# Kernel tuning notes

Measured on AMD Instinct MI355X. Metric: run time of the kernel, lower is better.

## Reference

```python
import jax, jax.numpy as jnp
import numpy as np

N = 80000
E = 1280000
EPS = 1e-5

def _lrelu(x):
    return jax.nn.leaky_relu(x, 0.01)

def _bn(h):
    # training-mode BatchNorm1d with batch size 1: stats over the node dim; affine is identity at init
    return (h - h.mean(0)) / jnp.sqrt(h.var(0) + EPS)

def _ln(h, g, b):
    m = h.mean(-1, keepdims=True)
    v = h.var(-1, keepdims=True)
    return (h - m) / jnp.sqrt(v + EPS) * g + b

def _gcn(h, w, b, src, dst, n):
    # PyG GCNConv: add self loops, symmetric deg^-1/2 normalization, aggregate at target
    hw = h @ w.T
    loop = jnp.arange(n, dtype=src.dtype)
    s = jnp.concatenate([src, loop])
    d = jnp.concatenate([dst, loop])
    deg = jax.ops.segment_sum(jnp.ones(d.shape, hw.dtype), d, num_segments=n)
    dinv = jnp.where(deg > 0, 1.0 / jnp.sqrt(deg), 0.0)
    msg = hw[s] * (dinv[s] * dinv[d])[:, None]  # [E+N, C]
    return jax.ops.segment_sum(msg, d, num_segments=n) + b

def _tnet(x, c1w, c1b, c2w, c2b, c3w, c3b, f1w, f1b, f2w, f2b, f3w, f3b):
    h = jax.nn.relu(x @ c1w.T + c1b)          # [N,64]  (source skips bn1)
    h = jax.nn.relu(_bn(h @ c2w.T + c2b))     # [N,128]
    h = jax.nn.relu(_bn(h @ c3w.T + c3b))     # [N,1024]
    g = h.max(0)                              # global max pool -> [1024]
    g = jax.nn.relu(g @ f1w.T + f1b)
    g = jax.nn.relu(g @ f2w.T + f2b)
    iden = jnp.array([1.0, 0.0, 0.0, 0.0, 1.0, 0.0, 0.0, 0.0, 1.0], x.dtype)
    g = g @ f3w.T + f3b + iden
    return g.reshape(3, 3)

def _forward(edge_index, x, tnet_c1_w, tnet_c1_b, tnet_c2_w, tnet_c2_b, tnet_c3_w, tnet_c3_b, tnet_fc1_w, tnet_fc1_b, tnet_fc2_w, tnet_fc2_b, tnet_fc3_w, tnet_fc3_b, conv1_w, conv1_b, g1_li_w, g1_li_b, g1_gcn_w, g1_gcn_b, g1_ln_g, g1_ln_b, conv2_w, conv2_b, g2_li_w, g2_li_b, g2_gcn_w, g2_gcn_b, g2_ln_g, g2_ln_b, conv3_w, conv3_b, out_w, out_b):
    src, dst = edge_index[0], edge_index[1]
    n = x.shape[0]
    T = _tnet(x, tnet_c1_w, tnet_c1_b, tnet_c2_w, tnet_c2_b, tnet_c3_w, tnet_c3_b, tnet_fc1_w, tnet_fc1_b, tnet_fc2_w, tnet_fc2_b, tnet_fc3_w, tnet_fc3_b)
    h0 = x @ T                                  # [N,3] spatial transform
    xg = _lrelu(h0 @ conv1_w.T + conv1_b)       # [N,64] (conv1d k=1 == per-node linear)
    # Gcn_Attention 1
    nf = _lrelu(xg @ g1_li_w.T + g1_li_b)
    nf2 = _lrelu(_gcn(nf, g1_gcn_w, g1_gcn_b, src, dst, n))
    h = _ln(jnp.concatenate([nf, nf2], 1), g1_ln_g, g1_ln_b)   # [N,128]
    h = _lrelu(h @ conv2_w.T + conv2_b)
    # Gcn_Attention 2
    nf = _lrelu(h @ g2_li_w.T + g2_li_b)
    nf2 = _lrelu(_gcn(nf, g2_gcn_w, g2_gcn_b, src, dst, n))
    h = _ln(jnp.concatenate([nf, nf2], 1), g2_ln_g, g2_ln_b)   # [N,256]
    h = jnp.concatenate([h, xg], 1)                            # [N,320]
    h = _lrelu(h @ conv3_w.T + conv3_b)                        # [N,256]
    pooled = h.mean(0)                                         # global mean pool (single graph)
    feat = jnp.concatenate([jnp.broadcast_to(pooled, (n, pooled.shape[0])), xg], 1)  # [N,320]
    return feat @ out_w.T + out_b                              # [N,4]

def setup_inputs():
    ki = iter(jax.random.split(jax.random.key(0), 32))
    def W(shape):
        return jax.random.normal(next(ki), shape, jnp.float32) * (1.0 / float(np.sqrt(shape[-1])))
    z = lambda n: jnp.zeros((n,), jnp.float32)
    o = lambda n: jnp.ones((n,), jnp.float32)
    inp = {}
    inp['x'] = jax.random.normal(next(ki), (N, 3), jnp.float32)
    inp['edge_index'] = jax.random.randint(next(ki), (2, E), 0, N, dtype=jnp.int32)
    inp['tnet_c1_w'] = W((64, 3)); inp['tnet_c1_b'] = z(64)
    inp['tnet_c2_w'] = W((128, 64)); inp['tnet_c2_b'] = z(128)
    inp['tnet_c3_w'] = W((1024, 128)); inp['tnet_c3_b'] = z(1024)
    inp['tnet_fc1_w'] = W((512, 1024)); inp['tnet_fc1_b'] = z(512)
    inp['tnet_fc2_w'] = W((256, 512)); inp['tnet_fc2_b'] = z(256)
    inp['tnet_fc3_w'] = W((9, 256)); inp['tnet_fc3_b'] = z(9)
    inp['conv1_w'] = W((64, 3)); inp['conv1_b'] = z(64)
    inp['g1_li_w'] = W((64, 64)); inp['g1_li_b'] = z(64)
    inp['g1_gcn_w'] = W((64, 64)); inp['g1_gcn_b'] = z(64)
    inp['g1_ln_g'] = o(128); inp['g1_ln_b'] = z(128)
    inp['conv2_w'] = W((128, 128)); inp['conv2_b'] = z(128)
    inp['g2_li_w'] = W((128, 128)); inp['g2_li_b'] = z(128)
    inp['g2_gcn_w'] = W((128, 128)); inp['g2_gcn_b'] = z(128)
    inp['g2_ln_g'] = o(256); inp['g2_ln_b'] = z(256)
    inp['conv3_w'] = W((256, 320)); inp['conv3_b'] = z(256)
    inp['out_w'] = W((4, 320)); inp['out_b'] = z(4)
    return inp

def reference(x, edge_index, tnet_c1_w, tnet_c1_b, tnet_c2_w, tnet_c2_b, tnet_c3_w, tnet_c3_b, tnet_fc1_w, tnet_fc1_b, tnet_fc2_w, tnet_fc2_b, tnet_fc3_w, tnet_fc3_b, conv1_w, conv1_b, g1_li_w, g1_li_b, g1_gcn_w, g1_gcn_b, g1_ln_g, g1_ln_b, conv2_w, conv2_b, g2_li_w, g2_li_b, g2_gcn_w, g2_gcn_b, g2_ln_g, g2_ln_b, conv3_w, conv3_b, out_w, out_b):
    return _forward(edge_index, x, tnet_c1_w, tnet_c1_b, tnet_c2_w, tnet_c2_b, tnet_c3_w, tnet_c3_b, tnet_fc1_w, tnet_fc1_b, tnet_fc2_w, tnet_fc2_b, tnet_fc3_w, tnet_fc3_b, conv1_w, conv1_b, g1_li_w, g1_li_b, g1_gcn_w, g1_gcn_b, g1_ln_g, g1_ln_b, conv2_w, conv2_b, g2_li_w, g2_li_b, g2_gcn_w, g2_gcn_b, g2_ln_g, g2_ln_b, conv3_w, conv3_b, out_w, out_b)
```

## Files before the change

### kernel.cpp

```cpp
#include <hip/hip_runtime.h>
#include <cstddef>

#define EPSV 1e-5f

typedef __attribute__((ext_vector_type(8))) short frag8;
typedef __attribute__((ext_vector_type(4))) float f32x4;

__device__ __forceinline__ float lrelu01(float v) { return v > 0.f ? v : 0.01f * v; }
__device__ __forceinline__ void atomAddF(float* p, float v) { unsafeAtomicAdd(p, v); }
__device__ __forceinline__ unsigned fkey(float f) {
    unsigned u = __float_as_uint(f);
    return (u & 0x80000000u) ? ~u : (u | 0x80000000u);
}
__device__ __forceinline__ unsigned short f2b(float f) {
    unsigned u = __float_as_uint(f);
    unsigned r = u + 0x7fffu + ((u >> 16) & 1u);
    return (unsigned short)(r >> 16);
}
__device__ __forceinline__ float b2f(unsigned short h) {
    return __uint_as_float(((unsigned)h) << 16);
}
__device__ __forceinline__ float blo(unsigned u) { return __uint_as_float(u << 16); }
__device__ __forceinline__ float bhi(unsigned u) { return __uint_as_float(u & 0xffff0000u); }

static inline unsigned cdivu(unsigned a, unsigned b) { return (a + b - 1) / b; }

__device__ __forceinline__ void gbar(unsigned* cnt, unsigned target) {
    __syncthreads();
    if (threadIdx.x == 0) {
        __threadfence();
        atomicAdd(cnt, 1u);
        while (atomicAdd(cnt, 0u) < target) { }
        __threadfence();
    }
    __syncthreads();
}


__device__ void degrank_body(int bid, const int* __restrict__ dst, int* __restrict__ deg,
                             int* __restrict__ rank, int E) {
    int e = bid * 256 + threadIdx.x;
    if (e < E) rank[e] = atomicAdd(&deg[dst[e]], 1);
}

__device__ void scan_local_body(int bid, const int* __restrict__ deg, int* __restrict__ startv,
                                int* __restrict__ bsum, float* __restrict__ dinv, int n) {
    __shared__ int t0[256];
    int tid = threadIdx.x;
    int i = bid * 256 + tid;
    int v = (i < n) ? deg[i] : 0;
    if (i < n) dinv[i] = rsqrtf((float)(v + 1));
    t0[tid] = v;
    __syncthreads();
    for (int o = 1; o < 256; o <<= 1) {
        int add = (tid >= o) ? t0[tid - o] : 0;
        __syncthreads();
        t0[tid] += add;
        __syncthreads();
    }
    if (i < n) startv[i] = t0[tid] - v;
    if (tid == 255) bsum[bid] = t0[255];
}

__device__ void scan_bsum_body(int* __restrict__ bsum, int nb) {
    __shared__ int t0[512];
    __shared__ int t1[512];
    int tid = threadIdx.x;
    int v0 = (tid < nb) ? bsum[tid] : 0;
    int v1 = (tid + 256 < nb) ? bsum[tid + 256] : 0;
    t0[tid] = v0; t0[tid + 256] = v1;
    __syncthreads();
    int* a = t0; int* b = t1;
    for (int o = 1; o < 512; o <<= 1) {
        b[tid]       = a[tid]       + ((tid >= o)       ? a[tid - o]       : 0);
        b[tid + 256] = a[tid + 256] + ((tid + 256 >= o) ? a[tid + 256 - o] : 0);
        __syncthreads();
        int* t = a; a = b; b = t;
    }
    if (tid < nb) bsum[tid] = a[tid] - v0;
    if (tid + 256 < nb) bsum[tid + 256] = a[tid + 256] - v1;
}

__device__ void fill_body(int bid, const int* __restrict__ src, const int* __restrict__ dst,
                          const int* __restrict__ rank, const int* __restrict__ startv,
                          const int* __restrict__ bsum, int* __restrict__ csr, int E) {
    int e = bid * 256 + threadIdx.x;
    if (e < E) {
        int d = dst[e];
        csr[startv[d] + bsum[d >> 8] + rank[e]] = src[e];
    }
}


__device__ void wconv_body(int bid, const float* __restrict__ s0, const float* __restrict__ s1,
                           const float* __restrict__ s2, const float* __restrict__ s3,
                           const float* __restrict__ s4, const float* __restrict__ s5,
                           const float* __restrict__ s6, const float* __restrict__ s7,
                           unsigned short* __restrict__ dst) {
    int t = bid * 256 + threadIdx.x;
    if (t >= 278528) return;
    const float* srcs[8] = {s0, s1, s2, s3, s4, s5, s6, s7};
    const int off[9] = {0, 8192, 139264, 143360, 147456, 163840, 180224, 196608, 278528};
    int seg = 0;
    while (t >= off[seg + 1]) ++seg;
    unsigned short v = f2b(srcs[seg][t - off[seg]]);
    if (seg == 1) {
        int li = t - 8192;
        int rch = li >> 7, k = li & 127;
        int cb = rch >> 7, r = rch & 127;
        int flat = ((r >> 4) * 4 + (k >> 5)) * 64 + ((k >> 3) & 3) * 16 + (r & 15);
        dst[8192 + cb * 16384 + flat * 8 + (k & 7)] = v;
    } else {
        dst[t] = v;
    }
}

__device__ void h1_body(int bid, const float* __restrict__ x, const float* __restrict__ w,
                        const float* __restrict__ b, unsigned short* __restrict__ h1, int n) {
    int node = bid * 256 + threadIdx.x;
    if (node >= n) return;
    float x0 = x[node * 3], x1 = x[node * 3 + 1], x2 = x[node * 3 + 2];
    unsigned short* o = h1 + (size_t)node * 64;
#pragma unroll
    for (int cp = 0; cp < 8; ++cp) {
        unsigned short tmp[8];
#pragma unroll
        for (int t = 0; t < 8; ++t) {
            int c = cp * 8 + t;
            float v = x0 * w[c * 3] + x1 * w[c * 3 + 1] + x2 * w[c * 3 + 2] + b[c];
            tmp[t] = f2b(fmaxf(v, 0.f));
        }
        *(float4*)(o + cp * 8) = *(float4*)tmp;
    }
}

__device__ void prebn_body(int bid, const float* __restrict__ z, const float* __restrict__ sum2,
                           const float* __restrict__ ss2, unsigned short* __restrict__ a3f,
                           int n16, float invn) {
    int t = bid * 256 + threadIdx.x;
    if (t >= n16) return;
    int row = t >> 4, cp = t & 15;
    int c = cp * 8;
    const float* src = z + (size_t)row * 128 + c;
    float4 v0 = *(const float4*)src;
    float4 v1 = *(const float4*)(src + 4);
    float vv[8] = {v0.x, v0.y, v0.z, v0.w, v1.x, v1.y, v1.z, v1.w};
    unsigned short o[8];
#pragma unroll
    for (int i = 0; i < 8; ++i) {
        float m = sum2[c + i] * invn;
        float var = ss2[c + i] * invn - m * m;
        o[i] = f2b(fmaxf((vv[i] - m) * rsqrtf(var + EPSV), 0.f));
    }
    int tile = row >> 7, r = row & 127;
    int flat = ((r >> 4) * 4 + (cp >> 2)) * 64 + (cp & 3) * 16 + (r & 15);
    *(float4*)(a3f + (size_t)tile * 16384 + flat * 8) = *(float4*)o;
}

enum { MF_BIAS = 1, MF_LRELU = 2, MF_DINV = 4, MF_STOREF = 8, MF_STOREB = 16,
       MF_STATS = 32, MF_COLSUM = 64 };

template <int BN, int MODE>
__device__ void mgemm_body(int bx, int by,
                           const unsigned short* __restrict__ A, int lda, int K,
                           const unsigned short* __restrict__ W,
                           const float* __restrict__ bias,
                           float* __restrict__ OutF, unsigned short* __restrict__ OutB, int ldo,
                           const float* __restrict__ dinv,
                           float* __restrict__ sum_o, float* __restrict__ ss_o,
                           unsigned* __restrict__ maxk_o) {
    constexpr int BM = 128;
    constexpr int LDT = 40;
    __shared__ unsigned short As[BM * LDT];
    __shared__ unsigned short Ws[BN * LDT];
    __shared__ float redS[2 * 128];
    __shared__ unsigned redM[128];

    const int tid = threadIdx.x;
    const int wid = tid >> 6, lane = tid & 63;
    const int quad = lane >> 4, lrow = lane & 15;
    const int bn0 = bx * BM;
    const int bc0 = by * BN;

    constexpr int NI = (BN == 128) ? 4 : 2;
    constexpr int NJ = 4;
    const int wm = (BN == 128) ? (wid & 1) * 64 : wid * 32;
    const int wn = (BN == 128) ? (wid >> 1) * 64 : 0;

    if (MODE & (MF_STATS | MF_COLSUM)) {
        for (int c = tid; c < BN; c += 256) {
            redS[c] = 0.f; redS[128 + c] = 0.f; redM[c] = 0u;
        }
    }

    f32x4 acc[NI][NJ] = {};

    for (int k0 = 0; k0 < K; k0 += 32) {
#pragma unroll
        for (int h = 0; h < 2; ++h) {
            int ch = tid + h * 256;
            int row = ch >> 2, cp = ch & 3;
            const unsigned short* src = A + (size_t)(bn0 + row) * lda + k0 + cp * 8;
            *(float4*)&As[row * LDT + cp * 8] = *(const float4*)src;
        }
#pragma unroll
        for (int h = 0; h < BN / 64; ++h) {
            int ch = tid + h * 256;
            int row = ch >> 2, cp = ch & 3;
            const unsigned short* src = W + (size_t)(bc0 + row) * K + k0 + cp * 8;
            *(float4*)&Ws[row * LDT + cp * 8] = *(const float4*)src;
        }
        __syncthreads();
        frag8 af[NI], bf[NJ];
#pragma unroll
        for (int i = 0; i < NI; ++i)
            af[i] = *(const frag8*)&As[(wm + i * 16 + lrow) * LDT + quad * 8];
#pragma unroll
        for (int j = 0; j < NJ; ++j)
            bf[j] = *(const frag8*)&Ws[(wn + j * 16 + lrow) * LDT + quad * 8];
#pragma unroll
        for (int i = 0; i < NI; ++i)
#pragma unroll
            for (int j = 0; j < NJ; ++j)
                acc[i][j] = __builtin_amdgcn_mfma_f32_16x16x32_bf16(af[i], bf[j], acc[i][j], 0, 0, 0);
        __syncthreads();
    }

#pragma unroll
    for (int j = 0; j < NJ; ++j) {
        const int col = bc0 + wn + j * 16 + lrow;
        float bv = (MODE & MF_BIAS) ? bias[col] : 0.f;
        float s = 0.f, q = 0.f, m = -3.4e38f;
#pragma unroll
        for (int i = 0; i < NI; ++i) {
            const int rowb = bn0 + wm + i * 16 + quad * 4;
#pragma unroll
            for (int r = 0; r < 4; ++r) {
                float t = acc[i][j][r] + bv;
                if (MODE & MF_LRELU) t = lrelu01(t);
                if (MODE & MF_DINV) t *= dinv[rowb + r];
                if (MODE & MF_STOREF) OutF[(size_t)(rowb + r) * ldo + col] = t;
                if (MODE & MF_STOREB) OutB[(size_t)(rowb + r) * ldo + col] = f2b(t);
                s += t; q += t * t; m = fmaxf(m, t);
            }
        }
        if (MODE & (MF_STATS | MF_COLSUM)) {
            s += __shfl_xor(s, 16); s += __shfl_xor(s, 32);
            if (MODE & MF_STATS) {
                q += __shfl_xor(q, 16); q += __shfl_xor(q, 32);
                m = fmaxf(m, __shfl_xor(m, 16)); m = fmaxf(m, __shfl_xor(m, 32));
            }
            if (quad == 0) {
                int lc = wn + j * 16 + lrow;
                atomicAdd(&redS[lc], s);
                if (MODE & MF_STATS) {
                    atomicAdd(&redS[128 + lc], q);
                    atomicMax(&redM[lc], fkey(m));
                }
            }
        }
    }
    if (MODE & (MF_STATS | MF_COLSUM)) {
        __syncthreads();
        for (int c = tid; c < BN; c += 256) {
            atomAddF(&sum_o[bc0 + c], redS[c]);
            if (MODE & MF_STATS) {
                atomAddF(&ss_o[bc0 + c], redS[128 + c]);
                atomicMax(&maxk_o[bc0 + c], redM[c]);
            }
        }
    }
}

template <int BN, int MODE, int SWAP>
__launch_bounds__(256)
__global__ void k_mgemm(const unsigned short* __restrict__ A, int lda, int K,
                        const unsigned short* __restrict__ W,
                        const float* __restrict__ bias,
                        float* __restrict__ OutF, unsigned short* __restrict__ OutB, int ldo,
                        const float* __restrict__ dinv,
                        float* __restrict__ sum_o, float* __restrict__ ss_o,
                        unsigned* __restrict__ maxk_o) {
    int bx = SWAP ? blockIdx.y : blockIdx.x;
    int by = SWAP ? blockIdx.x : blockIdx.y;
    mgemm_body<BN, MODE>(bx, by, A, lda, K, W, bias, OutF, OutB, ldo, dinv, sum_o, ss_o, maxk_o);
}

__device__ void z3_body(int bid,
                        const unsigned short* __restrict__ AF,
                        const unsigned short* __restrict__ WF,
                        const float* __restrict__ bias,
                        float* __restrict__ sum_o, float* __restrict__ ss_o,
                        unsigned* __restrict__ maxk_o, int ntiles) {
    const int tid = threadIdx.x;
    const int wid = tid >> 6, lane = tid & 63;
    const int quad = lane >> 4, lrow = lane & 15;

    int w = (bid & 7) * ntiles + (bid >> 3);
    const int tile = w >> 3;
    const int cb = w & 7;
    const unsigned short* At = AF + (size_t)tile * 16384;
    const unsigned short* Wt = WF + (size_t)cb * 16384;

    const int ar = (wid & 1) * 4;
    const int wc = (wid >> 1) * 4;
    f32x4 acc[4][4] = {};
#pragma unroll
    for (int kc = 0; kc < 4; ++kc) {
        frag8 af[4], bf[4];
#pragma unroll
        for (int i = 0; i < 4; ++i)
            af[i] = *(const frag8*)&At[(((ar + i) * 4 + kc) * 64 + lane) * 8];
#pragma unroll
        for (int j = 0; j < 4; ++j)
            bf[j] = *(const frag8*)&Wt[(((wc + j) * 4 + kc) * 64 + lane) * 8];
#pragma unroll
        for (int i = 0; i < 4; ++i)
#pragma unroll
            for (int j = 0; j < 4; ++j)
                acc[i][j] = __builtin_amdgcn_mfma_f32_16x16x32_bf16(af[i], bf[j], acc[i][j], 0, 0, 0);
    }

#pragma unroll
    for (int j = 0; j < 4; ++j) {
        int c = cb * 128 + (wc + j) * 16 + lrow;
        float bv = bias[c];
        float s = 0.f, q = 0.f, m = -3.4e38f;
#pragma unroll
        for (int i = 0; i < 4; ++i)
#pragma unroll
            for (int r = 0; r < 4; ++r) {
                float t = acc[i][j][r] + bv;
                s += t; q += t * t; m = fmaxf(m, t);
            }
        s += __shfl_xor(s, 16); s += __shfl_xor(s, 32);
        q += __shfl_xor(q, 16); q += __shfl_xor(q, 32);
        m = fmaxf(m, __shfl_xor(m, 16)); m = fmaxf(m, __shfl_xor(m, 32));
        if (quad == 0) {
            atomAddF(&sum_o[c], s);
            atomAddF(&ss_o[c], q);
            atomicMax(&maxk_o[c], fkey(m));
        }
    }
}


__launch_bounds__(256)
__global__ void FK1(const int* __restrict__ dst, int* __restrict__ deg, int* __restrict__ rank,
                    int E, int EB,
                    const float* s0, const float* s1, const float* s2, const float* s3,
                    const float* s4, const float* s5, const float* s6, const float* s7,
                    unsigned short* __restrict__ WB, int WCB,
                    const float* __restrict__ x, const float* __restrict__ c1w,
                    const float* __restrict__ c1b, unsigned short* __restrict__ B1, int n) {
    int b = blockIdx.x;
    if (b < EB) { degrank_body(b, dst, deg, rank, E); return; }
    b -= EB;
    if (b < WCB) { wconv_body(b, s0, s1, s2, s3, s4, s5, s6, s7, WB); return; }
    b -= WCB;
    h1_body(b, x, c1w, c1b, B1, n);
}

__launch_bounds__(256)
__global__ void FK2(const unsigned short* __restrict__ A, int lda, int K,
                    const unsigned short* __restrict__ W, const float* __restrict__ bias,
                    float* __restrict__ OutF, int ldo,
                    float* __restrict__ sum_o, float* __restrict__ ss_o,
                    unsigned* __restrict__ maxk_o, int GXz,
                    const int* __restrict__ deg, int* __restrict__ startv,
                    int* __restrict__ bsum, float* __restrict__ dinvv, int n) {
    if ((int)blockIdx.x < GXz)
        mgemm_body<128, (MF_BIAS | MF_STOREF | MF_STATS)>(
            blockIdx.x, 0, A, lda, K, W, bias, OutF, nullptr, ldo, nullptr, sum_o, ss_o, maxk_o);
    else
        scan_local_body(blockIdx.x - GXz, deg, startv, bsum, dinvv, n);
}

__launch_bounds__(256)
__global__ void FK3(const float* __restrict__ z, const float* __restrict__ sum2,
                    const float* __restrict__ ss2, unsigned short* __restrict__ a3f,
                    int n16, float invn, int PB, int* __restrict__ bsum, int nb) {
    if ((int)blockIdx.x < PB) prebn_body(blockIdx.x, z, sum2, ss2, a3f, n16, invn);
    else scan_bsum_body(bsum, nb);
}

__launch_bounds__(256)
__global__ void FK4(const unsigned short* __restrict__ AF, const unsigned short* __restrict__ WF,
                    const float* __restrict__ bias,
                    float* __restrict__ sum_o, float* __restrict__ ss_o,
                    unsigned* __restrict__ maxk_o, int NZ, int ntiles,
                    const int* __restrict__ src, const int* __restrict__ dst,
                    const int* __restrict__ rank, const int* __restrict__ startv,
                    const int* __restrict__ bsum, int* __restrict__ csr, int E) {
    int b = blockIdx.x;
    bool dofill = (b >= NZ);
    int idx = dofill ? (b - NZ) : b;
    if (dofill) fill_body(idx, src, dst, rank, startv, bsum, csr, E);
    else        z3_body(idx, AF, WF, bias, sum_o, ss_o, maxk_o, ntiles);
}

__launch_bounds__(256)
__global__ void k_tnet(const float* __restrict__ sum3, const float* __restrict__ ss3,
                       const unsigned* __restrict__ maxk,
                       const float* __restrict__ f1w, const float* __restrict__ f1b,
                       const float* __restrict__ f2w, const float* __restrict__ f2bias,
                       const float* __restrict__ f3w, const float* __restrict__ f3b,
                       float* __restrict__ a1, float* __restrict__ a2,
                       float* __restrict__ T9,
                       unsigned* __restrict__ cnt1, unsigned* __restrict__ cnt2, float invn) {
    __shared__ float g[1024];
    __shared__ float a1s[512];
    int tid = threadIdx.x;
    int bid = blockIdx.x;
    for (int c = tid; c < 1024; c += 256) {
        float m = sum3[c] * invn;
        float var = ss3[c] * invn - m * m;
        unsigned k = maxk[c];
        unsigned u = (k & 0x80000000u) ? (k & 0x7FFFFFFFu) : ~k;
        g[c] = fmaxf((__uint_as_float(u) - m) * rsqrtf(var + EPSV), 0.f);
    }
    __syncthreads();
    {
        int row = bid * 16 + (tid >> 4);
        int part = tid & 15;
        const float* w = f1w + (size_t)row * 1024 + part * 64;
        const float* gg = g + part * 64;
        float s = 0.f;
#pragma unroll 4
        for (int k = 0; k < 64; k += 4) {
            float4 wv = *(const float4*)(w + k);
            s = fmaf(wv.x, gg[k], s);
            s = fmaf(wv.y, gg[k + 1], s);
            s = fmaf(wv.z, gg[k + 2], s);
            s = fmaf(wv.w, gg[k + 3], s);
        }
        s += __shfl_xor(s, 1); s += __shfl_xor(s, 2);
        s += __shfl_xor(s, 4); s += __shfl_xor(s, 8);
        if (part == 0) a1[row] = fmaxf(s + f1b[row], 0.f);
    }
    gbar(cnt1, 32);
    a1s[tid] = a1[tid];
    a1s[tid + 256] = a1[tid + 256];
    __syncthreads();
    {
        int row = bid * 8 + (tid >> 5);
        int part = tid & 31;
        const float* w = f2w + (size_t)row * 512 + part * 16;
        const float* aa = a1s + part * 16;
        float s = 0.f;
#pragma unroll
        for (int k = 0; k < 16; k += 4) {
            float4 wv = *(const float4*)(w + k);
            s = fmaf(wv.x, aa[k], s);
            s = fmaf(wv.y, aa[k + 1], s);
            s = fmaf(wv.z, aa[k + 2], s);
            s = fmaf(wv.w, aa[k + 3], s);
        }
        s += __shfl_xor(s, 1); s += __shfl_xor(s, 2); s += __shfl_xor(s, 4);
        s += __shfl_xor(s, 8); s += __shfl_xor(s, 16);
        if (part == 0) a2[row] = fmaxf(s + f2bias[row], 0.f);
    }
    gbar(cnt2, 32);
    if (bid == 0 && tid < 144) {
        int r = tid >> 4, kk = (tid & 15) * 16;
        const float* wr = f3w + r * 256 + kk;
        float s = 0.f;
#pragma unroll
        for (int k = 0; k < 16; ++k) s = fmaf(wr[k], a2[kk + k], s);
        s += __shfl_xor(s, 1); s += __shfl_xor(s, 2);
        s += __shfl_xor(s, 4); s += __shfl_xor(s, 8);
        if ((tid & 15) == 0) {
            s += f3b[r];
            if (r == 0 || r == 4 || r == 8) s += 1.f;
            T9[r] = s;
        }
    }
}

template <int CH>
__launch_bounds__(256)
__global__ void k_gln(const int* __restrict__ startv, const int* __restrict__ bsum,
                      const int* __restrict__ degv,
                      const int* __restrict__ csr, const unsigned short* __restrict__ q,
                      const unsigned short* __restrict__ nf, const float* __restrict__ dinv,
                      const float* __restrict__ gcn_b, const float* __restrict__ lng,
                      const float* __restrict__ lnb, unsigned short* __restrict__ outp,
                      int ldo, int n, int nd) {
    constexpr int GRP = (CH == 64) ? 8 : 4;
    constexpr int PL  = 64 / GRP;
    constexpr int TT  = 16 / GRP;
    constexpr int CPL = CH / PL;
    const int wv = threadIdx.x >> 6, lane = threadIdx.x & 63;
    const int g = lane / PL, p = lane & (PL - 1);
    int node = blockIdx.x * 4 + wv;
    if (node >= n) return;

    const unsigned short* qp = q + (size_t)p * CPL;

    float acc[CPL];
    {
        uint4 v = *(const uint4*)(qp + (size_t)node * CH);
        unsigned sv[4] = {v.x, v.y, v.z, v.w};
        if (g == 0) {
#pragma unroll
            for (int d = 0; d < 4; ++d) { acc[2 * d] = blo(sv[d]); acc[2 * d + 1] = bhi(sv[d]); }
        } else {
#pragma unroll
            for (int k = 0; k < CPL; ++k) acc[k] = 0.f;
        }
    }

    int s0 = startv[node] + bsum[node >> 8], cnt = degv[node];
    const int* cs = csr + s0;
    int sidx[TT];
#pragma unroll
    for (int t = 0; t < TT; ++t) { int j = t * GRP + g; sidx[t] = (j < cnt) ? cs[j] : nd; }
    for (int j0 = 0; j0 < cnt; j0 += 16) {
        uint4 buf[TT];
#pragma unroll
        for (int t = 0; t < TT; ++t)
            buf[t] = *(const uint4*)(qp + (size_t)(unsigned)sidx[t] * CH);
#pragma unroll
        for (int t = 0; t < TT; ++t) {
            int j = j0 + 16 + t * GRP + g;
            sidx[t] = (j < cnt) ? cs[j] : nd;
        }
#pragma unroll
        for (int t = 0; t < TT; ++t) {
            unsigned bw[4] = {buf[t].x, buf[t].y, buf[t].z, buf[t].w};
#pragma unroll
            for (int d = 0; d < 4; ++d) {
                acc[2 * d] += blo(bw[d]);
                acc[2 * d + 1] += bhi(bw[d]);
            }
        }
    }

#pragma unroll
    for (int k = 0; k < CPL; ++k) {
#pragma unroll
        for (int off = PL; off < 64; off <<= 1) acc[k] += __shfl_xor(acc[k], off);
    }

    float di = dinv[node];
    float nv[CPL], bv[CPL];
    {
        uint4 v = *(const uint4*)(nf + (size_t)node * CH + p * CPL);
        unsigned sv[4] = {v.x, v.y, v.z, v.w};
#pragma unroll
        for (int d = 0; d < 4; ++d) { nv[2 * d] = blo(sv[d]); nv[2 * d + 1] = bhi(sv[d]); }
    }
    const float* gb = gcn_b + p * CPL;
#pragma unroll
    for (int k = 0; k < CPL; ++k) bv[k] = lrelu01(di * acc[k] + gb[k]);

    float s = 0.f, ss = 0.f;
#pragma unroll
    for (int k = 0; k < CPL; ++k) { s += nv[k] + bv[k]; ss += nv[k] * nv[k] + bv[k] * bv[k]; }
#pragma unroll
    for (int off = 32; off > 0; off >>= 1) { s += __shfl_xor(s, off); ss += __shfl_xor(ss, off); }
    const float inv = 1.f / (float)(GRP * 2 * CH);
    float mu = s * inv;
    float var = ss * inv - mu * mu;
    float rsg = rsqrtf(var + EPSV);

    unsigned short* orow = outp + (size_t)node * ldo;
    if (g == 0) {
        unsigned short tmp[CPL];
        const float* lg = lng + p * CPL; const float* lb = lnb + p * CPL;
#pragma unroll
        for (int k = 0; k < CPL; ++k) tmp[k] = f2b((nv[k] - mu) * rsg * lg[k] + lb[k]);
        *(uint4*)(orow + p * CPL) = *(uint4*)tmp;
    } else if (g == 1) {
        unsigned short tmp[CPL];
        const float* lg = lng + CH + p * CPL; const float* lb = lnb + CH + p * CPL;
#pragma unroll
        for (int k = 0; k < CPL; ++k) tmp[k] = f2b((bv[k] - mu) * rsg * lg[k] + lb[k]);
        *(uint4*)(orow + CH + p * CPL) = *(uint4*)tmp;
    }
}


__launch_bounds__(256)
__global__ void k_xg2(const float* __restrict__ x, const float* __restrict__ T9,
                      const float* __restrict__ w, const float* __restrict__ b,
                      const float* __restrict__ ow,
                      unsigned short* __restrict__ xg, float* __restrict__ xdot, int n) {
    __shared__ float owS[256];
    __shared__ float T9s[9];
    int tid = threadIdx.x;
    owS[tid] = ow[(tid >> 6) * 320 + 256 + (tid & 63)];
    if (tid < 9) T9s[tid] = T9[tid];
    __syncthreads();
    int node = blockIdx.x * 256 + tid;
    if (node >= n) return;
    float x0 = x[node * 3], x1 = x[node * 3 + 1], x2 = x[node * 3 + 2];
    float h0 = x0 * T9s[0] + x1 * T9s[3] + x2 * T9s[6];
    float h1 = x0 * T9s[1] + x1 * T9s[4] + x2 * T9s[7];
    float h2 = x0 * T9s[2] + x1 * T9s[5] + x2 * T9s[8];
    unsigned short* o = xg + (size_t)node * 320;
    float d0 = 0.f, d1 = 0.f, d2 = 0.f, d3 = 0.f;
#pragma unroll
    for (int cp = 0; cp < 8; ++cp) {
        unsigned short tmp[8];
#pragma unroll
        for (int t = 0; t < 8; ++t) {
            int c = cp * 8 + t;
            float v = lrelu01(h0 * w[c * 3] + h1 * w[c * 3 + 1] + h2 * w[c * 3 + 2] + b[c]);
            tmp[t] = f2b(v);
            d0 = fmaf(v, owS[c], d0);
            d1 = fmaf(v, owS[64 + c], d1);
            d2 = fmaf(v, owS[128 + c], d2);
            d3 = fmaf(v, owS[192 + c], d3);
        }
        *(float4*)(o + cp * 8) = *(float4*)tmp;
    }
    *(float4*)(xdot + (size_t)node * 4) = make_float4(d0, d1, d2, d3);
}

template <int BN>
__launch_bounds__(256)
__global__ void k_ligc(const unsigned short* __restrict__ A, int lda, int K,
                       const unsigned short* __restrict__ Wli, const float* __restrict__ bli,
                       const unsigned short* __restrict__ Wgc, const float* __restrict__ dinv,
                       unsigned short* __restrict__ NF, int ldnf,
                       unsigned short* __restrict__ Q, int ldq) {
    constexpr int BM = 128;
    constexpr int LDT = 40;
    constexpr int LDT2 = BN + 8;
    __shared__ unsigned short SA[BM * LDT2];
    __shared__ unsigned short Ws[BN * LDT];
    __shared__ unsigned short As[BM * LDT];

    const int tid = threadIdx.x;
    const int wid = tid >> 6, lane = tid & 63;
    const int quad = lane >> 4, lrow = lane & 15;
    const int bn0 = blockIdx.x * BM;
    constexpr int NI = (BN == 128) ? 4 : 2;
    constexpr int NJ = 4;
    const int wm = (BN == 128) ? (wid & 1) * 64 : wid * 32;
    const int wn = (BN == 128) ? (wid >> 1) * 64 : 0;

    {
        f32x4 acc[NI][NJ] = {};
        for (int k0 = 0; k0 < K; k0 += 32) {
#pragma unroll
            for (int h = 0; h < 2; ++h) {
                int ch = tid + h * 256;
                int row = ch >> 2, cp = ch & 3;
                *(float4*)&As[row * LDT + cp * 8] =
                    *(const float4*)(A + (size_t)(bn0 + row) * lda + k0 + cp * 8);
            }
#pragma unroll
            for (int h = 0; h < BN / 64; ++h) {
                int ch = tid + h * 256;
                int row = ch >> 2, cp = ch & 3;
                *(float4*)&Ws[row * LDT + cp * 8] =
                    *(const float4*)(Wli + (size_t)row * K + k0 + cp * 8);
            }
            __syncthreads();
            frag8 af[NI], bf[NJ];
#pragma unroll
            for (int i = 0; i < NI; ++i)
                af[i] = *(const frag8*)&As[(wm + i * 16 + lrow) * LDT + quad * 8];
#pragma unroll
            for (int j = 0; j < NJ; ++j)
                bf[j] = *(const frag8*)&Ws[(wn + j * 16 + lrow) * LDT + quad * 8];
#pragma unroll
            for (int i = 0; i < NI; ++i)
#pragma unroll
                for (int j = 0; j < NJ; ++j)
                    acc[i][j] = __builtin_amdgcn_mfma_f32_16x16x32_bf16(af[i], bf[j], acc[i][j], 0, 0, 0);
            __syncthreads();
        }
#pragma unroll
        for (int j = 0; j < NJ; ++j) {
            const int col = wn + j * 16 + lrow;
            float bv = bli[col];
#pragma unroll
            for (int i = 0; i < NI; ++i) {
                const int rowl = wm + i * 16 + quad * 4;
#pragma unroll
                for (int r = 0; r < 4; ++r) {
                    unsigned short h = f2b(lrelu01(acc[i][j][r] + bv));
                    NF[(size_t)(bn0 + rowl + r) * ldnf + col] = h;
                    SA[(rowl + r) * LDT2 + col] = h;
                }
            }
        }
        __syncthreads();
    }
    {
        f32x4 acc[NI][NJ] = {};
        for (int k0 = 0; k0 < BN; k0 += 32) {
#pragma unroll
            for (int h = 0; h < BN / 64; ++h) {
                int ch = tid + h * 256;
                int row = ch >> 2, cp = ch & 3;
                *(float4*)&Ws[row * LDT + cp * 8] =
                    *(const float4*)(Wgc + (size_t)row * BN + k0 + cp * 8);
            }
            __syncthreads();
            frag8 af[NI], bf[NJ];
#pragma unroll
            for (int i = 0; i < NI; ++i)
                af[i] = *(const frag8*)&SA[(wm + i * 16 + lrow) * LDT2 + k0 + quad * 8];
#pragma unroll
            for (int j = 0; j < NJ; ++j)
                bf[j] = *(const frag8*)&Ws[(wn + j * 16 + lrow) * LDT + quad * 8];
#pragma unroll
            for (int i = 0; i < NI; ++i)
#pragma unroll
                for (int j = 0; j < NJ; ++j)
                    acc[i][j] = __builtin_amdgcn_mfma_f32_16x16x32_bf16(af[i], bf[j], acc[i][j], 0, 0, 0);
            __syncthreads();
        }
#pragma unroll
        for (int j = 0; j < NJ; ++j) {
            const int col = wn + j * 16 + lrow;
#pragma unroll
            for (int i = 0; i < NI; ++i) {
                const int rowb = bn0 + wm + i * 16 + quad * 4;
#pragma unroll
                for (int r = 0; r < 4; ++r) {
                    float t = acc[i][j][r] * dinv[rowb + r];
                    Q[(size_t)(rowb + r) * ldq + col] = f2b(t);
                }
            }
        }
    }
}

__launch_bounds__(256)
__global__ void k_cligc(const unsigned short* __restrict__ A,
                        const unsigned short* __restrict__ Wcv, const float* __restrict__ bcv,
                        const unsigned short* __restrict__ Wli, const float* __restrict__ bli,
                        const unsigned short* __restrict__ Wgc, const float* __restrict__ dinv,
                        unsigned short* __restrict__ NF,
                        unsigned short* __restrict__ Q) {
    constexpr int LDT = 40;
    constexpr int LDT2 = 136;
    __shared__ unsigned short As[128 * LDT];
    __shared__ unsigned short Ws[128 * LDT];
    __shared__ unsigned short SA[128 * LDT2];

    const int tid = threadIdx.x;
    const int wid = tid >> 6, lane = tid & 63;
    const int quad = lane >> 4, lrow = lane & 15;
    const int bn0 = blockIdx.x * 128;
    const int wm = (wid & 1) * 64;
    const int wn = (wid >> 1) * 64;

    {
        f32x4 acc[4][4] = {};
        for (int k0 = 0; k0 < 128; k0 += 32) {
#pragma unroll
            for (int h = 0; h < 2; ++h) {
                int ch = tid + h * 256;
                int row = ch >> 2, cp = ch & 3;
                *(float4*)&As[row * LDT + cp * 8] =
                    *(const float4*)(A + (size_t)(bn0 + row) * 128 + k0 + cp * 8);
                *(float4*)&Ws[row * LDT + cp * 8] =
                    *(const float4*)(Wcv + (size_t)row * 128 + k0 + cp * 8);
            }
            __syncthreads();
            frag8 af[4], bf[4];
#pragma unroll
            for (int i = 0; i < 4; ++i)
                af[i] = *(const frag8*)&As[(wm + i * 16 + lrow) * LDT + quad * 8];
#pragma unroll
            for (int j = 0; j < 4; ++j)
                bf[j] = *(const frag8*)&Ws[(wn + j * 16 + lrow) * LDT + quad * 8];
#pragma unroll
            for (int i = 0; i < 4; ++i)
#pragma unroll
                for (int j = 0; j < 4; ++j)
                    acc[i][j] = __builtin_amdgcn_mfma_f32_16x16x32_bf16(af[i], bf[j], acc[i][j], 0, 0, 0);
            __syncthreads();
        }
#pragma unroll
        for (int j = 0; j < 4; ++j) {
            const int col = wn + j * 16 + lrow;
            float bv = bcv[col];
#pragma unroll
            for (int i = 0; i < 4; ++i) {
                const int rowl = wm + i * 16 + quad * 4;
#pragma unroll
                for (int r = 0; r < 4; ++r)
                    SA[(rowl + r) * LDT2 + col] = f2b(lrelu01(acc[i][j][r] + bv));
            }
        }
        __syncthreads();
    }
    {
        f32x4 acc[4][4] = {};
        for (int k0 = 0; k0 < 128; k0 += 32) {
#pragma unroll
            for (int h = 0; h < 2; ++h) {
                int ch = tid + h * 256;
                int row = ch >> 2, cp = ch & 3;
                *(float4*)&Ws[row * LDT + cp * 8] =
                    *(const float4*)(Wli + (size_t)row * 128 + k0 + cp * 8);
            }
            __syncthreads();
            frag8 af[4], bf[4];
#pragma unroll
            for (int i = 0; i < 4; ++i)
                af[i] = *(const frag8*)&SA[(wm + i * 16 + lrow) * LDT2 + k0 + quad * 8];
#pragma unroll
            for (int j = 0; j < 4; ++j)
                bf[j] = *(const frag8*)&Ws[(wn + j * 16 + lrow) * LDT + quad * 8];
#pragma unroll
            for (int i = 0; i < 4; ++i)
#pragma unroll
                for (int j = 0; j < 4; ++j)
                    acc[i][j] = __builtin_amdgcn_mfma_f32_16x16x32_bf16(af[i], bf[j], acc[i][j], 0, 0, 0);
            __syncthreads();
        }
#pragma unroll
        for (int j = 0; j < 4; ++j) {
            const int col = wn + j * 16 + lrow;
            float bv = bli[col];
#pragma unroll
            for (int i = 0; i < 4; ++i) {
                const int rowl = wm + i * 16 + quad * 4;
#pragma unroll
                for (int r = 0; r < 4; ++r) {
                    unsigned short h = f2b(lrelu01(acc[i][j][r] + bv));
                    NF[(size_t)(bn0 + rowl + r) * 128 + col] = h;
                    SA[(rowl + r) * LDT2 + col] = h;
                }
            }
        }
        __syncthreads();
    }
    {
        f32x4 acc[4][4] = {};
        for (int k0 = 0; k0 < 128; k0 += 32) {
#pragma unroll
            for (int h = 0; h < 2; ++h) {
                int ch = tid + h * 256;
                int row = ch >> 2, cp = ch & 3;
                *(float4*)&Ws[row * LDT + cp * 8] =
                    *(const float4*)(Wgc + (size_t)row * 128 + k0 + cp * 8);
            }
            __syncthreads();
            frag8 af[4], bf[4];
#pragma unroll
            for (int i = 0; i < 4; ++i)
                af[i] = *(const frag8*)&SA[(wm + i * 16 + lrow) * LDT2 + k0 + quad * 8];
#pragma unroll
            for (int j = 0; j < 4; ++j)
                bf[j] = *(const frag8*)&Ws[(wn + j * 16 + lrow) * LDT + quad * 8];
#pragma unroll
            for (int i = 0; i < 4; ++i)
#pragma unroll
                for (int j = 0; j < 4; ++j)
                    acc[i][j] = __builtin_amdgcn_mfma_f32_16x16x32_bf16(af[i], bf[j], acc[i][j], 0, 0, 0);
            __syncthreads();
        }
#pragma unroll
        for (int j = 0; j < 4; ++j) {
            const int col = wn + j * 16 + lrow;
#pragma unroll
            for (int i = 0; i < 4; ++i) {
                const int rowb = bn0 + wm + i * 16 + quad * 4;
#pragma unroll
                for (int r = 0; r < 4; ++r)
                    Q[(size_t)(rowb + r) * 128 + col] = f2b(acc[i][j][r] * dinv[rowb + r]);
            }
        }
    }
}

__global__ void k_out2(const float* __restrict__ xdot, const float* __restrict__ ow,
                       const float* __restrict__ ob, const float* __restrict__ pooled,
                       float* __restrict__ out, int n, float invn) {
    __shared__ float c4s[4];
    int tid = threadIdx.x;
    {
        int j = tid >> 6, lane = tid & 63;
        float s = 0.f;
        for (int c = lane; c < 256; c += 64) s += pooled[c] * invn * ow[j * 320 + c];
#pragma unroll
        for (int off = 32; off > 0; off >>= 1) s += __shfl_down(s, off);
        if (lane == 0) c4s[j] = s + ob[j];
    }
    __syncthreads();
    int node = blockIdx.x * 256 + tid;
    if (node >= n) return;
    float4 xd = *(const float4*)(xdot + (size_t)node * 4);
    *(float4*)(out + (size_t)node * 4) =
        make_float4(c4s[0] + xd.x, c4s[1] + xd.y, c4s[2] + xd.z, c4s[3] + xd.w);
}


extern "C" void kernel_launch(void* const* d_in, const int* in_sizes, int n_in,
                              void* d_out, int out_size, void* d_ws, size_t ws_size,
                              hipStream_t stream) {
    const float* x   = (const float*)d_in[0];
    const int*   ei  = (const int*)d_in[1];
    const float* c1w = (const float*)d_in[2];  const float* c1b = (const float*)d_in[3];
    const float* c2w = (const float*)d_in[4];  const float* c2b = (const float*)d_in[5];
    const float* c3w = (const float*)d_in[6];  const float* c3b = (const float*)d_in[7];
    const float* f1w = (const float*)d_in[8];  const float* f1b = (const float*)d_in[9];
    const float* f2w = (const float*)d_in[10]; const float* f2bp = (const float*)d_in[11];
    const float* f3w = (const float*)d_in[12]; const float* f3b = (const float*)d_in[13];
    const float* cv1w = (const float*)d_in[14]; const float* cv1b = (const float*)d_in[15];
    const float* li1w = (const float*)d_in[16]; const float* li1b = (const float*)d_in[17];
    const float* gc1w = (const float*)d_in[18]; const float* gc1b = (const float*)d_in[19];
    const float* ln1g = (const float*)d_in[20]; const float* ln1b = (const float*)d_in[21];
    const float* cv2w = (const float*)d_in[22]; const float* cv2b = (const float*)d_in[23];
    const float* li2w = (const float*)d_in[24]; const float* li2b = (const float*)d_in[25];
    const float* gc2w = (const float*)d_in[26]; const float* gc2b = (const float*)d_in[27];
    const float* ln2g = (const float*)d_in[28]; const float* ln2b = (const float*)d_in[29];
    const float* cv3w = (const float*)d_in[30]; const float* cv3b = (const float*)d_in[31];
    const float* ow  = (const float*)d_in[32]; const float* ob  = (const float*)d_in[33];
    float* out = (float*)d_out;

    const int N = in_sizes[0] / 3;
    const int E = in_sizes[1] / 2;
    const int* srcI = ei;
    const int* dstI = ei + E;

    char* base = (char*)d_ws;
    size_t off = 0;
    auto take = [&](size_t bytes) -> char* {
        char* p = base + off;
        off = (off + bytes + 255) & ~(size_t)255;
        return p;
    };
    int*   deg    = (int*)  take((size_t)N * 4);
    float* sm     = (float*)take(8192 * 4);
    float* dinv   = (float*)take((size_t)N * 4);
    int*   startv = (int*)  take((size_t)N * 4);
    int*   rank   = (int*)  take((size_t)E * 4);
    int*   csr    = (int*)  take((size_t)E * 4);
    int*   bsum   = (int*)  take(512 * 4);
    unsigned short* WB = (unsigned short*)take(278528 * 2);
    unsigned short* H  = (unsigned short*)take((size_t)N * 320 * 2);
    float* F1 = (float*)take((size_t)N * 128 * 4);
    unsigned short* B1 = (unsigned short*)take((size_t)N * 64 * 2);
    unsigned short* B2 = (unsigned short*)take(((size_t)N * 128 + 128) * 2);
    unsigned short* B3 = (unsigned short*)take((size_t)N * 128 * 2);
    float* XD = (float*)take((size_t)N * 4 * 4);

    unsigned short* c2wb  = WB + 0;
    unsigned short* c3wf  = WB + 8192;
    unsigned short* li1wb = WB + 139264;
    unsigned short* gc1wb = WB + 143360;
    unsigned short* cv2wb = WB + 147456;
    unsigned short* li2wb = WB + 163840;
    unsigned short* gc2wb = WB + 180224;
    unsigned short* cv3wb = WB + 196608;

    float* sum2 = sm + 0;    float* ss2 = sm + 128;
    float* sum3 = sm + 256;  float* ss3 = sm + 1280;
    unsigned* maxk = (unsigned*)(sm + 2304);
    float* pooled = sm + 3328;
    unsigned* dmax = (unsigned*)(sm + 3584);
    unsigned* cnt1 = (unsigned*)(sm + 3712);
    unsigned* cnt2 = (unsigned*)(sm + 3713);
    float* T9  = sm + 3968;
    float* a1  = sm + 5120;
    float* a2  = sm + 5760;

    const float invn = 1.0f / (float)N;
    const dim3 blk(256);
    const unsigned GX = (unsigned)(N / 128);
    const unsigned NB = cdivu((unsigned)N, 256);
    const unsigned EB = cdivu((unsigned)E, 256);
    const unsigned WCB = cdivu(278528u, 256);
    const unsigned PB = cdivu((unsigned)N * 16, 256);
    const unsigned NZ = 8 * GX;

    size_t degpad = ((size_t)N * 4 + 255) & ~(size_t)255;
    hipMemsetAsync(deg, 0, degpad + 3720 * 4, stream);
    hipMemsetAsync(B2 + (size_t)N * 128, 0, 256, stream);

    FK1<<<EB + WCB + NB, blk, 0, stream>>>(dstI, deg, rank, E, (int)EB,
                                           c2w, c3w, li1w, gc1w, cv2w, li2w, gc2w, cv3w,
                                           WB, (int)WCB, x, c1w, c1b, B1, N);
    FK2<<<GX + NB, blk, 0, stream>>>(B1, 64, 64, c2wb, c2b, F1, 128,
                                     sum2, ss2, dmax, (int)GX, deg, startv, bsum, dinv, N);
    FK3<<<PB + 1, blk, 0, stream>>>(F1, sum2, ss2, B2, N * 16, invn, (int)PB, bsum, (int)NB);
    FK4<<<NZ + EB, blk, 0, stream>>>(B2, c3wf, c3b, sum3, ss3, maxk, (int)NZ, (int)GX,
                                     srcI, dstI, rank, startv, bsum, csr, E);
    k_tnet<<<32, blk, 0, stream>>>(sum3, ss3, maxk, f1w, f1b, f2w, f2bp, f3w, f3b,
                                   a1, a2, T9, cnt1, cnt2, invn);
    k_xg2<<<NB, blk, 0, stream>>>(x, T9, cv1w, cv1b, ow, H + 256, XD, N);

    k_ligc<64><<<GX, blk, 0, stream>>>(H + 256, 320, 64, li1wb, li1b, gc1wb, dinv, B1, 64, B2, 64);
    k_gln<64><<<cdivu((unsigned)N, 4), blk, 0, stream>>>(
        startv, bsum, deg, csr, B2, B1, dinv, gc1b, ln1g, ln1b, B3, 128, N, 2 * N);

    k_cligc<<<GX, blk, 0, stream>>>(B3, cv2wb, cv2b, li2wb, li2b, gc2wb, dinv, B3, B2);
    k_gln<128><<<cdivu((unsigned)N, 4), blk, 0, stream>>>(
        startv, bsum, deg, csr, B2, B3, dinv, gc2b, ln2g, ln2b, H, 320, N, N);

    k_mgemm<128, (MF_BIAS | MF_LRELU | MF_COLSUM), 1><<<dim3(2, GX), blk, 0, stream>>>(
        H, 320, 320, cv3wb, cv3b, nullptr, nullptr, 0, nullptr, pooled, nullptr, nullptr);

    k_out2<<<NB, blk, 0, stream>>>(XD, ow, ob, pooled, out, N, invn);
}
```

Baseline: 490.4 us.

## Fuse tnet with xg and conv3 with output via in-kernel spin barriers

Merges the tnet MLP kernel with the per-node xg kernel, and the final conv3 GEMM with the output kernel. In each merged kernel the consumer blocks spin on an atomic counter until the producer blocks have finished. This removes two kernel launches and the idle gaps between them. FK1 also interleaves degree/rank blocks with weight-conversion/h1 blocks to balance the work mix. The spin-wait depends on producer blocks being scheduled ahead of the spinning consumers, which risks deadlock or lost occupancy if the dispatch order differs.

```diff
diff --git a/kernel.cpp b/kernel.cpp
--- a/kernel.cpp
+++ b/kernel.cpp
@@ -272,20 +272,6 @@
     }
 }
 
-template <int BN, int MODE, int SWAP>
-__launch_bounds__(256)
-__global__ void k_mgemm(const unsigned short* __restrict__ A, int lda, int K,
-                        const unsigned short* __restrict__ W,
-                        const float* __restrict__ bias,
-                        float* __restrict__ OutF, unsigned short* __restrict__ OutB, int ldo,
-                        const float* __restrict__ dinv,
-                        float* __restrict__ sum_o, float* __restrict__ ss_o,
-                        unsigned* __restrict__ maxk_o) {
-    int bx = SWAP ? blockIdx.y : blockIdx.x;
-    int by = SWAP ? blockIdx.x : blockIdx.y;
-    mgemm_body<BN, MODE>(bx, by, A, lda, K, W, bias, OutF, OutB, ldo, dinv, sum_o, ss_o, maxk_o);
-}
-
 __device__ void z3_body(int bid,
                         const unsigned short* __restrict__ AF,
                         const unsigned short* __restrict__ WF,
@@ -354,11 +340,26 @@
                     const float* __restrict__ x, const float* __restrict__ c1w,
                     const float* __restrict__ c1b, unsigned short* __restrict__ B1, int n) {
     int b = blockIdx.x;
-    if (b < EB) { degrank_body(b, dst, deg, rank, E); return; }
-    b -= EB;
-    if (b < WCB) { wconv_body(b, s0, s1, s2, s3, s4, s5, s6, s7, WB); return; }
-    b -= WCB;
-    h1_body(b, x, c1w, c1b, B1, n);
+    int AUX = WCB + (int)((n + 255) >> 8);
+    int mn = (EB < AUX) ? EB : AUX;
+    bool doaux;
+    int idx;
+    if (b < 2 * mn) {
+        doaux = (b & 1) != 0;
+        idx = b >> 1;
+    } else if (EB > AUX) {
+        doaux = false;
+        idx = b - AUX;
+    } else {
+        doaux = true;
+        idx = b - EB;
+    }
+    if (doaux) {
+        if (idx < WCB) wconv_body(idx, s0, s1, s2, s3, s4, s5, s6, s7, WB);
+        else h1_body(idx - WCB, x, c1w, c1b, B1, n);
+    } else {
+        degrank_body(idx, dst, deg, rank, E);
+    }
 }
 
 __launch_bounds__(256)
@@ -400,81 +401,126 @@
 }
 
 __launch_bounds__(256)
-__global__ void k_tnet(const float* __restrict__ sum3, const float* __restrict__ ss3,
-                       const unsigned* __restrict__ maxk,
-                       const float* __restrict__ f1w, const float* __restrict__ f1b,
-                       const float* __restrict__ f2w, const float* __restrict__ f2bias,
-                       const float* __restrict__ f3w, const float* __restrict__ f3b,
-                       float* __restrict__ a1, float* __restrict__ a2,
-                       float* __restrict__ T9,
-                       unsigned* __restrict__ cnt1, unsigned* __restrict__ cnt2, float invn) {
-    __shared__ float g[1024];
-    __shared__ float a1s[512];
+__global__ void k_tnetxg(const float* __restrict__ sum3, const float* __restrict__ ss3,
+                         const unsigned* __restrict__ maxk,
+                         const float* __restrict__ f1w, const float* __restrict__ f1b,
+                         const float* __restrict__ f2w, const float* __restrict__ f2bias,
+                         const float* __restrict__ f3w, const float* __restrict__ f3b,
+                         float* __restrict__ a1, float* __restrict__ a2,
+                         float* __restrict__ T9,
+                         unsigned* __restrict__ cnt1, unsigned* __restrict__ cnt2,
+                         unsigned* __restrict__ cnt4, float invn,
+                         const float* __restrict__ x, const float* __restrict__ w,
+                         const float* __restrict__ b, const float* __restrict__ ow,
+                         unsigned short* __restrict__ xg, float* __restrict__ xdot, int n) {
     int tid = threadIdx.x;
     int bid = blockIdx.x;
-    for (int c = tid; c < 1024; c += 256) {
-        float m = sum3[c] * invn;
-        float var = ss3[c] * invn - m * m;
-        unsigned k = maxk[c];
-        unsigned u = (k & 0x80000000u) ? (k & 0x7FFFFFFFu) : ~k;
-        g[c] = fmaxf((__uint_as_float(u) - m) * rsqrtf(var + EPSV), 0.f);
+    if (bid < 32) {
+        __shared__ float g[1024];
+        __shared__ float a1s[512];
+        for (int c = tid; c < 1024; c += 256) {
+            float m = sum3[c] * invn;
+            float var = ss3[c] * invn - m * m;
+            unsigned k = maxk[c];
+            unsigned u = (k & 0x80000000u) ? (k & 0x7FFFFFFFu) : ~k;
+            g[c] = fmaxf((__uint_as_float(u) - m) * rsqrtf(var + EPSV), 0.f);
+        }
+        __syncthreads();
+        {
+            int row = bid * 16 + (tid >> 4);
+            int part = tid & 15;
+            const float* wv0 = f1w + (size_t)row * 1024 + part * 64;
+            const float* gg = g + part * 64;
+            float s = 0.f;
+#pragma unroll 4
+            for (int k = 0; k < 64; k += 4) {
+                float4 wv = *(const float4*)(wv0 + k);
+                s = fmaf(wv.x, gg[k], s);
+                s = fmaf(wv.y, gg[k + 1], s);
+                s = fmaf(wv.z, gg[k + 2], s);
+                s = fmaf(wv.w, gg[k + 3], s);
+            }
+            s += __shfl_xor(s, 1); s += __shfl_xor(s, 2);
+            s += __shfl_xor(s, 4); s += __shfl_xor(s, 8);
+            if (part == 0) a1[row] = fmaxf(s + f1b[row], 0.f);
+        }
+        gbar(cnt1, 32);
+        a1s[tid] = a1[tid];
+        a1s[tid + 256] = a1[tid + 256];
+        __syncthreads();
+        {
+            int row = bid * 8 + (tid >> 5);
+            int part = tid & 31;
+            const float* wv0 = f2w + (size_t)row * 512 + part * 16;
+            const float* aa = a1s + part * 16;
+            float s = 0.f;
+#pragma unroll
+            for (int k = 0; k < 16; k += 4) {
+                float4 wv = *(const float4*)(wv0 + k);
+                s = fmaf(wv.x, aa[k], s);
+                s = fmaf(wv.y, aa[k + 1], s);
+                s = fmaf(wv.z, aa[k + 2], s);
+                s = fmaf(wv.w, aa[k + 3], s);
+            }
+            s += __shfl_xor(s, 1); s += __shfl_xor(s, 2); s += __shfl_xor(s, 4);
+            s += __shfl_xor(s, 8); s += __shfl_xor(s, 16);
+            if (part == 0) a2[row] = fmaxf(s + f2bias[row], 0.f);
+        }
+        gbar(cnt2, 32);
+        if (bid == 0) {
+            if (tid < 144) {
+                int r = tid >> 4, kk = (tid & 15) * 16;
+                const float* wr = f3w + r * 256 + kk;
+                float s = 0.f;
+#pragma unroll
+                for (int k = 0; k < 16; ++k) s = fmaf(wr[k], a2[kk + k], s);
+                s += __shfl_xor(s, 1); s += __shfl_xor(s, 2);
+                s += __shfl_xor(s, 4); s += __shfl_xor(s, 8);
+                if ((tid & 15) == 0) {
+                    s += f3b[r];
+                    if (r == 0 || r == 4 || r == 8) s += 1.f;
+                    T9[r] = s;
+                }
+            }
+            __syncthreads();
+            if (tid == 0) { __threadfence(); atomicAdd(cnt4, 1u); }
+        }
+        return;
+    }
+    if (tid == 0) {
+        while (atomicAdd(cnt4, 0u) < 1u) { }
+        __threadfence();
     }
     __syncthreads();
-    {
-        int row = bid * 16 + (tid >> 4);
-        int part = tid & 15;
-        const float* w = f1w + (size_t)row * 1024 + part * 64;
-        const float* gg = g + part * 64;
-        float s = 0.f;
-#pragma unroll 4
-        for (int k = 0; k < 64; k += 4) {
-            float4 wv = *(const float4*)(w + k);
-            s = fmaf(wv.x, gg[k], s);
-            s = fmaf(wv.y, gg[k + 1], s);
-            s = fmaf(wv.z, gg[k + 2], s);
-            s = fmaf(wv.w, gg[k + 3], s);
-        }
-        s += __shfl_xor(s, 1); s += __shfl_xor(s, 2);
-        s += __shfl_xor(s, 4); s += __shfl_xor(s, 8);
-        if (part == 0) a1[row] = fmaxf(s + f1b[row], 0.f);
-    }
-    gbar(cnt1, 32);
-    a1s[tid] = a1[tid];
-    a1s[tid + 256] = a1[tid + 256];
+    __shared__ float owS[256];
+    __shared__ float T9s[9];
+    owS[tid] = ow[(tid >> 6) * 320 + 256 + (tid & 63)];
+    if (tid < 9) T9s[tid] = T9[tid];
     __syncthreads();
-    {
-        int row = bid * 8 + (tid >> 5);
-        int part = tid & 31;
-        const float* w = f2w + (size_t)row * 512 + part * 16;
-        const float* aa = a1s + part * 16;
-        float s = 0.f;
-#pragma unroll
-        for (int k = 0; k < 16; k += 4) {
-            float4 wv = *(const float4*)(w + k);
-            s = fmaf(wv.x, aa[k], s);
-            s = fmaf(wv.y, aa[k + 1], s);
-            s = fmaf(wv.z, aa[k + 2], s);
-            s = fmaf(wv.w, aa[k + 3], s);
-        }
-        s += __shfl_xor(s, 1); s += __shfl_xor(s, 2); s += __shfl_xor(s, 4);
-        s += __shfl_xor(s, 8); s += __shfl_xor(s, 16);
-        if (part == 0) a2[row] = fmaxf(s + f2bias[row], 0.f);
-    }
-    gbar(cnt2, 32);
-    if (bid == 0 && tid < 144) {
-        int r = tid >> 4, kk = (tid & 15) * 16;
-        const float* wr = f3w + r * 256 + kk;
-        float s = 0.f;
-#pragma unroll
-        for (int k = 0; k < 16; ++k) s = fmaf(wr[k], a2[kk + k], s);
-        s += __shfl_xor(s, 1); s += __shfl_xor(s, 2);
-        s += __shfl_xor(s, 4); s += __shfl_xor(s, 8);
-        if ((tid & 15) == 0) {
-            s += f3b[r];
-            if (r == 0 || r == 4 || r == 8) s += 1.f;
-            T9[r] = s;
-        }
-    }
+    int node = (bid - 32) * 256 + tid;
+    if (node >= n) return;
+    float x0 = x[node * 3], x1 = x[node * 3 + 1], x2 = x[node * 3 + 2];
+    float h0 = x0 * T9s[0] + x1 * T9s[3] + x2 * T9s[6];
+    float h1 = x0 * T9s[1] + x1 * T9s[4] + x2 * T9s[7];
+    float h2 = x0 * T9s[2] + x1 * T9s[5] + x2 * T9s[8];
+    unsigned short* o = xg + (size_t)node * 320;
+    float d0 = 0.f, d1 = 0.f, d2 = 0.f, d3 = 0.f;
+#pragma unroll
+    for (int cp = 0; cp < 8; ++cp) {
+        unsigned short tmp[8];
+#pragma unroll
+        for (int t = 0; t < 8; ++t) {
+            int c = cp * 8 + t;
+            float v = lrelu01(h0 * w[c * 3] + h1 * w[c * 3 + 1] + h2 * w[c * 3 + 2] + b[c]);
+            tmp[t] = f2b(v);
+            d0 = fmaf(v, owS[c], d0);
+            d1 = fmaf(v, owS[64 + c], d1);
+            d2 = fmaf(v, owS[128 + c], d2);
+            d3 = fmaf(v, owS[192 + c], d3);
+        }
+        *(float4*)(o + cp * 8) = *(float4*)tmp;
+    }
+    *(float4*)(xdot + (size_t)node * 4) = make_float4(d0, d1, d2, d3);
 }
 
 template <int CH>
@@ -580,44 +626,6 @@
     }
 }
 
-
-__launch_bounds__(256)
-__global__ void k_xg2(const float* __restrict__ x, const float* __restrict__ T9,
-                      const float* __restrict__ w, const float* __restrict__ b,
-                      const float* __restrict__ ow,
-                      unsigned short* __restrict__ xg, float* __restrict__ xdot, int n) {
-    __shared__ float owS[256];
-    __shared__ float T9s[9];
-    int tid = threadIdx.x;
-    owS[tid] = ow[(tid >> 6) * 320 + 256 + (tid & 63)];
-    if (tid < 9) T9s[tid] = T9[tid];
-    __syncthreads();
-    int node = blockIdx.x * 256 + tid;
-    if (node >= n) return;
-    float x0 = x[node * 3], x1 = x[node * 3 + 1], x2 = x[node * 3 + 2];
-    float h0 = x0 * T9s[0] + x1 * T9s[3] + x2 * T9s[6];
-    float h1 = x0 * T9s[1] + x1 * T9s[4] + x2 * T9s[7];
-    float h2 = x0 * T9s[2] + x1 * T9s[5] + x2 * T9s[8];
-    unsigned short* o = xg + (size_t)node * 320;
-    float d0 = 0.f, d1 = 0.f, d2 = 0.f, d3 = 0.f;
-#pragma unroll
-    for (int cp = 0; cp < 8; ++cp) {
-        unsigned short tmp[8];
-#pragma unroll
-        for (int t = 0; t < 8; ++t) {
-            int c = cp * 8 + t;
-            float v = lrelu01(h0 * w[c * 3] + h1 * w[c * 3 + 1] + h2 * w[c * 3 + 2] + b[c]);
-            tmp[t] = f2b(v);
-            d0 = fmaf(v, owS[c], d0);
-            d1 = fmaf(v, owS[64 + c], d1);
-            d2 = fmaf(v, owS[128 + c], d2);
-            d3 = fmaf(v, owS[192 + c], d3);
-        }
-        *(float4*)(o + cp * 8) = *(float4*)tmp;
-    }
-    *(float4*)(xdot + (size_t)node * 4) = make_float4(d0, d1, d2, d3);
-}
-
 template <int BN>
 __launch_bounds__(256)
 __global__ void k_ligc(const unsigned short* __restrict__ A, int lda, int K,
@@ -873,11 +881,29 @@
     }
 }
 
-__global__ void k_out2(const float* __restrict__ xdot, const float* __restrict__ ow,
-                       const float* __restrict__ ob, const float* __restrict__ pooled,
-                       float* __restrict__ out, int n, float invn) {
+__launch_bounds__(256)
+__global__ void k_cvout(const unsigned short* __restrict__ H, const unsigned short* __restrict__ W,
+                        const float* __restrict__ bias, float* __restrict__ pooled, int GXv,
+                        const float* __restrict__ xdot, const float* __restrict__ ow,
+                        const float* __restrict__ ob, float* __restrict__ out, int n, float invn,
+                        unsigned* __restrict__ cnt5) {
+    int b = blockIdx.x;
+    int NC = 2 * GXv;
+    int tid = threadIdx.x;
+    if (b < NC) {
+        mgemm_body<128, (MF_BIAS | MF_LRELU | MF_COLSUM)>(
+            b >> 1, b & 1, H, 320, 320, W, bias, nullptr, nullptr, 0, nullptr,
+            pooled, nullptr, nullptr);
+        __syncthreads();
+        if (tid == 0) { __threadfence(); atomicAdd(cnt5, 1u); }
+        return;
+    }
+    if (tid == 0) {
+        while (atomicAdd(cnt5, 0u) < (unsigned)NC) { }
+        __threadfence();
+    }
+    __syncthreads();
     __shared__ float c4s[4];
-    int tid = threadIdx.x;
     {
         int j = tid >> 6, lane = tid & 63;
         float s = 0.f;
@@ -887,7 +913,7 @@
         if (lane == 0) c4s[j] = s + ob[j];
     }
     __syncthreads();
-    int node = blockIdx.x * 256 + tid;
+    int node = (b - NC) * 256 + tid;
     if (node >= n) return;
     float4 xd = *(const float4*)(xdot + (size_t)node * 4);
     *(float4*)(out + (size_t)node * 4) =
@@ -961,6 +987,8 @@
     unsigned* dmax = (unsigned*)(sm + 3584);
     unsigned* cnt1 = (unsigned*)(sm + 3712);
     unsigned* cnt2 = (unsigned*)(sm + 3713);
+    unsigned* cnt4 = (unsigned*)(sm + 3714);
+    unsigned* cnt5 = (unsigned*)(sm + 3715);
     float* T9  = sm + 3968;
     float* a1  = sm + 5120;
     float* a2  = sm + 5760;
@@ -986,9 +1014,9 @@
     FK3<<<PB + 1, blk, 0, stream>>>(F1, sum2, ss2, B2, N * 16, invn, (int)PB, bsum, (int)NB);
     FK4<<<NZ + EB, blk, 0, stream>>>(B2, c3wf, c3b, sum3, ss3, maxk, (int)NZ, (int)GX,
                                      srcI, dstI, rank, startv, bsum, csr, E);
-    k_tnet<<<32, blk, 0, stream>>>(sum3, ss3, maxk, f1w, f1b, f2w, f2bp, f3w, f3b,
-                                   a1, a2, T9, cnt1, cnt2, invn);
-    k_xg2<<<NB, blk, 0, stream>>>(x, T9, cv1w, cv1b, ow, H + 256, XD, N);
+    k_tnetxg<<<32 + NB, blk, 0, stream>>>(sum3, ss3, maxk, f1w, f1b, f2w, f2bp, f3w, f3b,
+                                          a1, a2, T9, cnt1, cnt2, cnt4, invn,
+                                          x, cv1w, cv1b, ow, H + 256, XD, N);
 
     k_ligc<64><<<GX, blk, 0, stream>>>(H + 256, 320, 64, li1wb, li1b, gc1wb, dinv, B1, 64, B2, 64);
     k_gln<64><<<cdivu((unsigned)N, 4), blk, 0, stream>>>(
@@ -998,8 +1026,6 @@
     k_gln<128><<<cdivu((unsigned)N, 4), blk, 0, stream>>>(
         startv, bsum, deg, csr, B2, B3, dinv, gc2b, ln2g, ln2b, H, 320, N, N);
 
-    k_mgemm<128, (MF_BIAS | MF_LRELU | MF_COLSUM), 1><<<dim3(2, GX), blk, 0, stream>>>(
-        H, 320, 320, cv3wb, cv3b, nullptr, nullptr, 0, nullptr, pooled, nullptr, nullptr);
-
-    k_out2<<<NB, blk, 0, stream>>>(XD, ow, ob, pooled, out, N, invn);
-}
+    k_cvout<<<2 * GX + NB, blk, 0, stream>>>(H, cv3wb, cv3b, pooled, (int)GX,
+                                             XD, ow, ob, out, N, invn, cnt5);
+}
```

After: 591.4 us. 20.6% more time.
